# Kernel optimization log

Measured on AMD Instinct MI355X. Metric: run time of the kernel, lower is better.

The kernel has to match this reference:

```python
import jax, jax.numpy as jnp
import numpy as np

NEG = 1.0e12  # large subtractive penalty from the original code


def setup_inputs() -> dict:
    key = jax.random.key(0)
    k1, k2, k3, k4 = jax.random.split(key, 4)
    b, q_len, ns, ls, e = 8, 512, 64, 128, 256
    q = jax.random.normal(k1, (b, q_len, e), dtype=jnp.float32)
    k = jax.random.normal(k2, (b, ns, ls, e), dtype=jnp.float32)
    v = jax.random.normal(k3, (b, ns, ls, e), dtype=jnp.float32)
    mask = jax.random.randint(k4, (b, ns, ls), 0, 2) > 0  # bool, True = keep
    return {"q": q, "k": k, "v": v, "mask": mask}


def reference(q, k, v, mask):
    # scores: (b, q_len, num_snippet, len_snippet)
    attn = jnp.einsum("bqe,bsle->bqsl", q, k)
    # original: attn = attn - (~mask) * 1e12, broadcast over q_len
    penalty = jnp.where(mask, 0.0, NEG).astype(attn.dtype)  # (b, s, l)
    attn = attn - penalty[:, None, :, :]
    attn = jax.nn.softmax(attn, axis=3)  # softmax within each snippet
    # weighted sum over len_snippet -> (b, q_len, num_snippet, e_dim)
    out = jnp.einsum("bqsl,bsle->bqse", attn, v)
    return out
```

## Files before the change

kernel.cpp:

```cpp
#include <hip/hip_runtime.h>

typedef _Float16 half8  __attribute__((ext_vector_type(8)));
typedef float    f32x4  __attribute__((ext_vector_type(4)));
typedef unsigned int u32;

#define QLEN  512
#define NS    64
#define LS    128
#define EDIM  256

__device__ __forceinline__ void block_sync_lds() {
    asm volatile("s_waitcnt lgkmcnt(0)" ::: "memory");
    __builtin_amdgcn_s_barrier();
    asm volatile("" ::: "memory");
}

__device__ __forceinline__ half8 cvt8(f32x4 a, f32x4 b) {
    half8 h;
    h[0]=(_Float16)a[0]; h[1]=(_Float16)a[1]; h[2]=(_Float16)a[2]; h[3]=(_Float16)a[3];
    h[4]=(_Float16)b[0]; h[5]=(_Float16)b[1]; h[6]=(_Float16)b[2]; h[7]=(_Float16)b[3];
    return h;
}

#define KLOAD(lt) do {                                                        \
  _Pragma("unroll") for (int it = 0; it < 4; ++it) {                          \
    int f = it * 2048 + tid * 8; int r = f >> 8; int e0 = f & 255;            \
    const float* src = kbase + (size_t)((lt) * 32 + r) * EDIM + e0;           \
    kr[2*it]   = *(const f32x4*)src;                                          \
    kr[2*it+1] = *(const f32x4*)(src + 4); } } while (0)

#define KSTORE(bi) do {                                                       \
  _Pragma("unroll") for (int it = 0; it < 4; ++it) {                          \
    int f = it * 2048 + tid * 8; int r = f >> 8; int e0 = f & 255;            \
    half8 h = cvt8(kr[2*it], kr[2*it+1]);                                     \
    *(half8*)(kvbuf + (bi) * 16384 + r * 512 + ((e0 * 2) ^ ((r & 7) << 4))) = h; } } while (0)

#define VLOAD(lt) do {                                                        \
  const float* vb0 = vbase + (size_t)((lt) * 32 + vlh * 16) * EDIM + vp;      \
  _Pragma("unroll") for (int i = 0; i < 16; ++i) {                            \
    vrL[i] = vb0[(size_t)i * EDIM];                                           \
    vrH[i] = vb0[(size_t)i * EDIM + 128]; } } while (0)

#define VSTORE(p) do {                                                        \
  _Pragma("unroll") for (int jj = 0; jj < 2; ++jj) {                          \
    half8 h0, h1;                                                             \
    _Pragma("unroll") for (int j = 0; j < 8; ++j) {                           \
      h0[j] = (_Float16)vrL[jj*8+j]; h1[j] = (_Float16)vrH[jj*8+j]; }         \
    int u   = vlh * 2 + jj;                                                   \
    int a0  = ((p) & 1) * 16384 + vp * 64 + ((u ^ ((vp >> 1) & 3)) * 16);     \
    *(half8*)(kvbuf + a0)        = h0;                                        \
    *(half8*)(kvbuf + a0 + 8192) = h1; } } while (0)

#define MAKE_PF(sacc, pf) do {                                                \
  u32 pk0[8], pk1[8];                                                         \
  _Pragma("unroll") for (int t = 0; t < 8; ++t) {                             \
    pk0[t] = __builtin_bit_cast(u32, __builtin_amdgcn_cvt_pkrtz(sacc[t][0], sacc[t][1])); \
    pk1[t] = __builtin_bit_cast(u32, __builtin_amdgcn_cvt_pkrtz(sacc[t][2], sacc[t][3])); \
  }                                                                           \
  _Pragma("unroll") for (int lt = 0; lt < 4; ++lt) {                          \
    u32 zx = sel2 ? pk0[2*lt+1] : pk0[2*lt];                                  \
    u32 zy = sel2 ? pk1[2*lt+1] : pk1[2*lt];                                  \
    u32 wx = sel2 ? pk0[2*lt]   : pk0[2*lt+1];                                \
    u32 wy = sel2 ? pk1[2*lt]   : pk1[2*lt+1];                                \
    u32 az0 = (u32)__shfl((int)zx, s0l, 64), az1 = (u32)__shfl((int)zy, s0l, 64); \
    u32 aw0 = (u32)__shfl((int)wx, s0l, 64), aw1 = (u32)__shfl((int)wy, s0l, 64); \
    u32 bz0 = (u32)__shfl((int)zx, s1l, 64), bz1 = (u32)__shfl((int)zy, s1l, 64); \
    u32 bw0 = (u32)__shfl((int)wx, s1l, 64), bw1 = (u32)__shfl((int)wy, s1l, 64); \
    union { u32 u[4]; half8 h; } t_;                                          \
    t_.u[0] = useZ ? az0 : aw0;  t_.u[1] = useZ ? az1 : aw1;                  \
    t_.u[2] = useZ ? bz0 : bw0;  t_.u[3] = useZ ? bz1 : bw1;                  \
    pf[lt] = t_.h; } } while (0)

#define PV2(lt) do {                                                          \
  const unsigned char* vb = kvbuf + ((lt) & 1) * 16384;                       \
  _Pragma("unroll") for (int et = 0; et < 16; ++et) {                         \
    int e = et * 16 + c;                                                      \
    half8 vf = *(const half8*)(vb + (size_t)e * 64 + ((g ^ ((c >> 1) & 3)) * 16)); \
    oaccA[et] = __builtin_amdgcn_mfma_f32_16x16x32_f16(vf, pfA[lt], oaccA[et], 0, 0, 0); \
    oaccB[et] = __builtin_amdgcn_mfma_f32_16x16x32_f16(vf, pfB[lt], oaccB[et], 0, 0, 0); } \
  } while (0)

__global__ __launch_bounds__(256, 2)
void DotAttn_20083267076209_kernel(const float* __restrict__ qg,
                                   const float* __restrict__ kg,
                                   const float* __restrict__ vg,
                                   const int*   __restrict__ maskg,
                                   float*       __restrict__ outg)
{
    __shared__ __align__(16) unsigned char kvbuf[32768];

    const int tid  = threadIdx.x;
    const int lane = tid & 63;
    const int c    = lane & 15;
    const int g    = lane >> 4;
    const int vp   = tid & 127;
    const int vlh  = tid >> 7;
    const int w    = tid >> 6;

    const bool sel2 = (g >= 2);
    const bool useZ = (g == 0) || (g == 3);
    const int  s0l  = c + ((g & 1) << 5);
    const int  s1l  = s0l + 16;

    const int bid = blockIdx.x;
    const int xcd = bid & 7;
    const int qt  = (bid >> 3) & 3;
    const int b   = (bid >> 5) & 7;
    const int s   = (bid >> 8) * 8 + xcd;

    const float* kbase  = kg + (size_t)(b * NS + s) * LS * EDIM;
    const float* vbase  = vg + (size_t)(b * NS + s) * LS * EDIM;
    const float* qbaseA = qg + ((size_t)b * QLEN + (size_t)qt * 128 + (size_t)w * 16) * EDIM;
    const float* qbaseB = qbaseA + (size_t)64 * EDIM;

    const int* mb = maskg + (b * NS + s) * LS;
    int mraw0 = mb[lane];
    int mraw1 = mb[64 + lane];

    f32x4 kr[8];
    KLOAD(0);

    half8 qfA[8], qfB[8];
#pragma unroll
    for (int ks = 0; ks < 8; ++ks) {
        const float* pA = qbaseA + (size_t)c * EDIM + ks * 32 + g * 8;
        const float* pB = qbaseB + (size_t)c * EDIM + ks * 32 + g * 8;
        qfA[ks] = cvt8(*(const f32x4*)pA, *(const f32x4*)(pA + 4));
        qfB[ks] = cvt8(*(const f32x4*)pB, *(const f32x4*)(pB + 4));
    }

    unsigned long long m0 = __ballot(mraw0 != 0);
    unsigned long long m1 = __ballot(mraw1 != 0);

    float vrL[16], vrH[16];

    f32x4 saccA[8], saccB[8];
#pragma unroll
    for (int t = 0; t < 8; ++t) {
        saccA[t] = (f32x4){0.f, 0.f, 0.f, 0.f};
        saccB[t] = (f32x4){0.f, 0.f, 0.f, 0.f};
    }

#pragma unroll
    for (int lt = 0; lt < 4; ++lt) {
        KSTORE(lt & 1);
        if (lt < 3) KLOAD(lt + 1);
        else        VLOAD(0);
        block_sync_lds();
        const unsigned char* kb = kvbuf + (lt & 1) * 16384;
#pragma unroll
        for (int lb = 0; lb < 2; ++lb) {
            int row  = lb * 16 + c;
            int base = row * 512;
            int sw   = (c & 7) << 4;
#pragma unroll
            for (int ks = 0; ks < 8; ++ks) {
                half8 kf = *(const half8*)(kb + base + ((ks * 64 + g * 16) ^ sw));
                saccA[lt * 2 + lb] =
                    __builtin_amdgcn_mfma_f32_16x16x32_f16(kf, qfA[ks], saccA[lt * 2 + lb], 0, 0, 0);
                saccB[lt * 2 + lb] =
                    __builtin_amdgcn_mfma_f32_16x16x32_f16(kf, qfB[ks], saccB[lt * 2 + lb], 0, 0, 0);
            }
        }
    }

#pragma unroll
    for (int t = 0; t < 8; ++t) {
        unsigned bits = (unsigned)(((t < 4 ? m0 : m1) >> ((t & 3) * 16 + 4 * g)) & 0xFull);
#pragma unroll
        for (int r = 0; r < 4; ++r)
            if (!((bits >> r) & 1)) { saccA[t][r] = -1e30f; saccB[t][r] = -1e30f; }
    }

#pragma unroll
    for (int tile = 0; tile < 2; ++tile) {
        f32x4* sc = tile ? saccB : saccA;
        float m = sc[0][0];
#pragma unroll
        for (int t = 0; t < 8; ++t)
#pragma unroll
            for (int r = 0; r < 4; ++r) m = fmaxf(m, sc[t][r]);
        m = fmaxf(m, __shfl_xor(m, 16, 64));
        m = fmaxf(m, __shfl_xor(m, 32, 64));
        float sum = 0.f;
#pragma unroll
        for (int t = 0; t < 8; ++t)
#pragma unroll
            for (int r = 0; r < 4; ++r) {
                float p = __expf(sc[t][r] - m);
                sc[t][r] = p;
                sum += p;
            }
        sum += __shfl_xor(sum, 16, 64);
        sum += __shfl_xor(sum, 32, 64);
        float inv = 1.f / sum;
#pragma unroll
        for (int t = 0; t < 8; ++t)
#pragma unroll
            for (int r = 0; r < 4; ++r) sc[t][r] *= inv;
    }

    half8 pfA[4], pfB[4];
    MAKE_PF(saccA, pfA);
    MAKE_PF(saccB, pfB);

    f32x4 oaccA[16], oaccB[16];
#pragma unroll
    for (int et = 0; et < 16; ++et) {
        oaccA[et] = (f32x4){0.f, 0.f, 0.f, 0.f};
        oaccB[et] = (f32x4){0.f, 0.f, 0.f, 0.f};
    }

    VSTORE(0);
    VLOAD(1);
    block_sync_lds();
    PV2(0);
    VSTORE(1);
    VLOAD(2);
    block_sync_lds();
    PV2(1);
    VSTORE(2);
    VLOAD(3);
    block_sync_lds();
    PV2(2);
    VSTORE(3);
    block_sync_lds();
    PV2(3);

    float* obA = outg + (((size_t)b * QLEN + (size_t)qt * 128 + w * 16 + c) * NS + s) * EDIM + 4 * g;
    float* obB = obA + (size_t)64 * NS * EDIM;
#pragma unroll
    for (int et = 0; et < 16; ++et) {
        *(f32x4*)(obA + et * 16) = oaccA[et];
        *(f32x4*)(obB + et * 16) = oaccB[et];
    }
}

extern "C" void kernel_launch(void* const* d_in, const int* in_sizes, int n_in,
                              void* d_out, int out_size, void* d_ws, size_t ws_size,
                              hipStream_t stream) {
    const float* q    = (const float*)d_in[0];
    const float* k    = (const float*)d_in[1];
    const float* v    = (const float*)d_in[2];
    const int*   mask = (const int*)d_in[3];
    float* out = (float*)d_out;
    dim3 grid(2048);
    dim3 block(256);
    hipLaunchKernelGGL(DotAttn_20083267076209_kernel, grid, block, 0, stream,
                       q, k, v, mask, out);
}
```

Baseline: 141.7 us.

## Stage all K tiles up front and batch V tile loads with fewer barriers

Doubles the LDS buffer to 64KB so all four K tiles are converted and stored before the QK phase, which then needs only one barrier. V tiles are loaded two at a time into two register sets and written into four LDS slots, cutting the barrier count during PV. The goal is more global loads in flight and less synchronisation stall. In exchange it raises LDS use per block and adds register pressure, which may hurt occupancy under the two-blocks-per-CU bound.

Measured after the change: 156.3 us. 10.3% more time.

```diff
diff --git a/kernel.cpp b/kernel.cpp
--- a/kernel.cpp
+++ b/kernel.cpp
@@ -22,32 +22,32 @@
     return h;
 }
 
-#define KLOAD(lt) do {                                                        \
+#define KLOAD(dst, lt) do {                                                   \
   _Pragma("unroll") for (int it = 0; it < 4; ++it) {                          \
     int f = it * 2048 + tid * 8; int r = f >> 8; int e0 = f & 255;            \
     const float* src = kbase + (size_t)((lt) * 32 + r) * EDIM + e0;           \
-    kr[2*it]   = *(const f32x4*)src;                                          \
-    kr[2*it+1] = *(const f32x4*)(src + 4); } } while (0)
-
-#define KSTORE(bi) do {                                                       \
+    dst[2*it]   = *(const f32x4*)src;                                         \
+    dst[2*it+1] = *(const f32x4*)(src + 4); } } while (0)
+
+#define KSTORE(sv, lt) do {                                                   \
   _Pragma("unroll") for (int it = 0; it < 4; ++it) {                          \
     int f = it * 2048 + tid * 8; int r = f >> 8; int e0 = f & 255;            \
-    half8 h = cvt8(kr[2*it], kr[2*it+1]);                                     \
-    *(half8*)(kvbuf + (bi) * 16384 + r * 512 + ((e0 * 2) ^ ((r & 7) << 4))) = h; } } while (0)
-
-#define VLOAD(lt) do {                                                        \
+    half8 h = cvt8(sv[2*it], sv[2*it+1]);                                     \
+    *(half8*)(kvbuf + (lt) * 16384 + r * 512 + ((e0 * 2) ^ ((r & 7) << 4))) = h; } } while (0)
+
+#define VLOAD(dL, dH, lt) do {                                                \
   const float* vb0 = vbase + (size_t)((lt) * 32 + vlh * 16) * EDIM + vp;      \
   _Pragma("unroll") for (int i = 0; i < 16; ++i) {                            \
-    vrL[i] = vb0[(size_t)i * EDIM];                                           \
-    vrH[i] = vb0[(size_t)i * EDIM + 128]; } } while (0)
-
-#define VSTORE(p) do {                                                        \
+    dL[i] = vb0[(size_t)i * EDIM];                                            \
+    dH[i] = vb0[(size_t)i * EDIM + 128]; } } while (0)
+
+#define VSTORE(dL, dH, p) do {                                                \
   _Pragma("unroll") for (int jj = 0; jj < 2; ++jj) {                          \
     half8 h0, h1;                                                             \
     _Pragma("unroll") for (int j = 0; j < 8; ++j) {                           \
-      h0[j] = (_Float16)vrL[jj*8+j]; h1[j] = (_Float16)vrH[jj*8+j]; }         \
+      h0[j] = (_Float16)dL[jj*8+j]; h1[j] = (_Float16)dH[jj*8+j]; }           \
     int u   = vlh * 2 + jj;                                                   \
-    int a0  = ((p) & 1) * 16384 + vp * 64 + ((u ^ ((vp >> 1) & 3)) * 16);     \
+    int a0  = (p) * 16384 + vp * 64 + ((u ^ ((vp >> 1) & 3)) * 16);           \
     *(half8*)(kvbuf + a0)        = h0;                                        \
     *(half8*)(kvbuf + a0 + 8192) = h1; } } while (0)
 
@@ -72,7 +72,7 @@
     pf[lt] = t_.h; } } while (0)
 
 #define PV2(lt) do {                                                          \
-  const unsigned char* vb = kvbuf + ((lt) & 1) * 16384;                       \
+  const unsigned char* vb = kvbuf + (lt) * 16384;                             \
   _Pragma("unroll") for (int et = 0; et < 16; ++et) {                         \
     int e = et * 16 + c;                                                      \
     half8 vf = *(const half8*)(vb + (size_t)e * 64 + ((g ^ ((c >> 1) & 3)) * 16)); \
@@ -87,7 +87,7 @@
                                    const int*   __restrict__ maskg,
                                    float*       __restrict__ outg)
 {
-    __shared__ __align__(16) unsigned char kvbuf[32768];
+    __shared__ __align__(16) unsigned char kvbuf[65536];
 
     const int tid  = threadIdx.x;
     const int lane = tid & 63;
@@ -117,8 +117,9 @@
     int mraw0 = mb[lane];
     int mraw1 = mb[64 + lane];
 
-    f32x4 kr[8];
-    KLOAD(0);
+    f32x4 kr0[8], kr1[8];
+    KLOAD(kr0, 0);
+    KLOAD(kr1, 1);
 
     half8 qfA[8], qfB[8];
 #pragma unroll
@@ -132,7 +133,14 @@
     unsigned long long m0 = __ballot(mraw0 != 0);
     unsigned long long m1 = __ballot(mraw1 != 0);
 
-    float vrL[16], vrH[16];
+    KSTORE(kr0, 0);
+    KLOAD(kr0, 2);
+    KSTORE(kr1, 1);
+    KLOAD(kr1, 3);
+    KSTORE(kr0, 2);
+    KSTORE(kr1, 3);
+
+    block_sync_lds();
 
     f32x4 saccA[8], saccB[8];
 #pragma unroll
@@ -141,13 +149,11 @@
         saccB[t] = (f32x4){0.f, 0.f, 0.f, 0.f};
     }
 
+    float vr0L[16], vr0H[16], vr1L[16], vr1H[16];
+
 #pragma unroll
     for (int lt = 0; lt < 4; ++lt) {
-        KSTORE(lt & 1);
-        if (lt < 3) KLOAD(lt + 1);
-        else        VLOAD(0);
-        block_sync_lds();
-        const unsigned char* kb = kvbuf + (lt & 1) * 16384;
+        const unsigned char* kb = kvbuf + lt * 16384;
 #pragma unroll
         for (int lb = 0; lb < 2; ++lb) {
             int row  = lb * 16 + c;
@@ -162,6 +168,8 @@
                     __builtin_amdgcn_mfma_f32_16x16x32_f16(kf, qfB[ks], saccB[lt * 2 + lb], 0, 0, 0);
             }
         }
+        if (lt == 2) { VLOAD(vr0L, vr0H, 0); }
+        if (lt == 3) { VLOAD(vr1L, vr1H, 1); }
     }
 
 #pragma unroll
@@ -211,20 +219,18 @@
         oaccB[et] = (f32x4){0.f, 0.f, 0.f, 0.f};
     }
 
-    VSTORE(0);
-    VLOAD(1);
+    block_sync_lds();
+    VSTORE(vr0L, vr0H, 0);
+    VSTORE(vr1L, vr1H, 1);
+    VLOAD(vr0L, vr0H, 2);
+    VLOAD(vr1L, vr1H, 3);
     block_sync_lds();
     PV2(0);
-    VSTORE(1);
-    VLOAD(2);
-    block_sync_lds();
     PV2(1);
-    VSTORE(2);
-    VLOAD(3);
+    VSTORE(vr0L, vr0H, 2);
+    VSTORE(vr1L, vr1H, 3);
     block_sync_lds();
     PV2(2);
-    VSTORE(3);
-    block_sync_lds();
     PV2(3);
 
     float* obA = outg + (((size_t)b * QLEN + (size_t)qt * 128 + w * 16 + c) * NS + s) * EDIM + 4 * g;
```
